# Optimization experiments

Measured on AMD Instinct MI355X. Metric: run time of the kernel, lower is better.

The kernel has to match this reference:

```python
import jax, jax.numpy as jnp
import numpy as np

HIDDEN = 1024
HEADS = 16
HEAD_DIM = HIDDEN // HEADS
EPS = 1e-5


def _layernorm(x, w, b):
    mu = jnp.mean(x, axis=-1, keepdims=True)
    var = jnp.mean(jnp.square(x - mu), axis=-1, keepdims=True)
    return (x - mu) * jax.lax.rsqrt(var + EPS) * w + b


def setup_inputs() -> dict:
    key = jax.random.key(0)
    ks = jax.random.split(key, 8)
    D = HIDDEN
    x = jax.random.normal(ks[0], (4, 4096, D), dtype=jnp.float32)
    s = 0.02
    return {
        "x": x,
        "qkv_w": jax.random.normal(ks[1], (3 * D, D), jnp.float32) * s,
        "qkv_b": jnp.zeros((3 * D,), jnp.float32),
        "proj_w": jax.random.normal(ks[2], (D, D), jnp.float32) * s,
        "proj_b": jnp.zeros((D,), jnp.float32),
        "ln1_w": jnp.ones((D,), jnp.float32),
        "ln1_b": jnp.zeros((D,), jnp.float32),
        "ln2_w": jnp.ones((D,), jnp.float32),
        "ln2_b": jnp.zeros((D,), jnp.float32),
        "mlp_w1": jax.random.normal(ks[3], (4 * D, D), jnp.float32) * s,
        "mlp_b1": jnp.zeros((4 * D,), jnp.float32),
        "mlp_w2": jax.random.normal(ks[4], (D, 4 * D), jnp.float32) * s,
        "mlp_b2": jnp.zeros((D,), jnp.float32),
    }


def reference(x, qkv_w, qkv_b, proj_w, proj_b, ln1_w, ln1_b, ln2_w, ln2_b,
              mlp_w1, mlp_b1, mlp_w2, mlp_b2):
    B, L, D = x.shape
    h = _layernorm(x, ln1_w, ln1_b)
    qkv = (h @ qkv_w.T + qkv_b).reshape(B, L, 3, HEADS, HEAD_DIM)
    q, k, v = qkv[:, :, 0], qkv[:, :, 1], qkv[:, :, 2]  # (B, L, H, hd)
    # NOTE: faithful to source - NO (L,H) transpose, so attention mixes
    # across the head axis per token: scores shape (B, L, H, H).
    attn = jnp.einsum('blhd,blgd->blhg', q, k) / np.sqrt(HEAD_DIM).astype(np.float32)
    attn = jax.nn.softmax(attn, axis=-1)
    out = jnp.einsum('blhg,blgd->blhd', attn, v).reshape(B, L, D)
    out = out @ proj_w.T + proj_b
    x = x + out
    h2 = _layernorm(x, ln2_w, ln2_b)
    mlp = jax.nn.gelu(h2 @ mlp_w1.T + mlp_b1, approximate=False) @ mlp_w2.T + mlp_b2
    return x + mlp
```

## Files before the change

kernel.cpp:

```cpp
#include <hip/hip_runtime.h>
#include <cstdint>
#include <cmath>


#define NTOK   16384
#define DMODEL 1024

typedef __bf16 bf16x8 __attribute__((ext_vector_type(8)));
typedef float  f32x4  __attribute__((ext_vector_type(4)));
typedef unsigned int __attribute__((address_space(1))) as1_uint;
typedef unsigned int __attribute__((address_space(3))) as3_uint;

__device__ __forceinline__ unsigned short f2bf(float f) {
    unsigned int u = __builtin_bit_cast(unsigned int, f);
    u += 0x7fffu + ((u >> 16) & 1u);
    return (unsigned short)(u >> 16);
}
__device__ __forceinline__ float bf2f(unsigned short s) {
    unsigned int u = ((unsigned int)s) << 16;
    return __builtin_bit_cast(float, u);
}

__device__ __forceinline__ void g2l16(const unsigned short* g, unsigned short* l) {
    __builtin_amdgcn_global_load_lds((const as1_uint*)g, (as3_uint*)l, 16, 0, 0);
}

__global__ __launch_bounds__(256) void cast_f32_bf16(
    const float4* __restrict__ in, ushort4* __restrict__ out, int n4) {
    int i = blockIdx.x * 256 + threadIdx.x;
    if (i < n4) {
        float4 v = in[i];
        ushort4 o;
        o.x = f2bf(v.x); o.y = f2bf(v.y); o.z = f2bf(v.z); o.w = f2bf(v.w);
        out[i] = o;
    }
}

__global__ __launch_bounds__(256) void ln_cast(
    const float* __restrict__ x, const float* __restrict__ w,
    const float* __restrict__ b, unsigned short* __restrict__ out) {
    int tok = blockIdx.x;
    int t   = threadIdx.x;
    float4 v = ((const float4*)x)[tok * 256 + t];
    float s  = v.x + v.y + v.z + v.w;
    float ss = v.x * v.x + v.y * v.y + v.z * v.z + v.w * v.w;
    #pragma unroll
    for (int off = 32; off > 0; off >>= 1) {
        s  += __shfl_down(s, off);
        ss += __shfl_down(ss, off);
    }
    __shared__ float red[8];
    int wave = t >> 6;
    if ((t & 63) == 0) { red[wave * 2] = s; red[wave * 2 + 1] = ss; }
    __syncthreads();
    s  = red[0] + red[2] + red[4] + red[6];
    ss = red[1] + red[3] + red[5] + red[7];
    float mu  = s * (1.0f / 1024.0f);
    float var = ss * (1.0f / 1024.0f) - mu * mu;
    float rs  = rsqrtf(var + 1e-5f);
    float4 wv = ((const float4*)w)[t];
    float4 bv = ((const float4*)b)[t];
    ushort4 o;
    o.x = f2bf((v.x - mu) * rs * wv.x + bv.x);
    o.y = f2bf((v.y - mu) * rs * wv.y + bv.y);
    o.z = f2bf((v.z - mu) * rs * wv.z + bv.z);
    o.w = f2bf((v.w - mu) * rs * wv.w + bv.w);
    ((ushort4*)out)[tok * 256 + t] = o;
}

__global__ __launch_bounds__(256) void attn_heads(
    const unsigned short* __restrict__ qkv, unsigned short* __restrict__ out) {
    __shared__ float sQ[1024], sK[1024], sV[1024];
    __shared__ float sS[256];
    int tok = blockIdx.x;
    int t   = threadIdx.x;
    const unsigned short* base = qkv + (size_t)tok * 3072;
    for (int i = t; i < 1024; i += 256) {
        sQ[i] = bf2f(base[i]);
        sK[i] = bf2f(base[1024 + i]);
        sV[i] = bf2f(base[2048 + i]);
    }
    __syncthreads();
    {
        int h = t >> 4, g = t & 15;
        float s = 0.0f;
        #pragma unroll
        for (int d = 0; d < 64; ++d) s += sQ[h * 64 + d] * sK[g * 64 + d];
        sS[h * 16 + g] = s * 0.125f;
    }
    __syncthreads();
    if (t < 16) {
        float mx = -1e30f;
        for (int g = 0; g < 16; ++g) mx = fmaxf(mx, sS[t * 16 + g]);
        float sum = 0.0f;
        for (int g = 0; g < 16; ++g) {
            float e = expf(sS[t * 16 + g] - mx);
            sS[t * 16 + g] = e;
            sum += e;
        }
        float inv = 1.0f / sum;
        for (int g = 0; g < 16; ++g) sS[t * 16 + g] *= inv;
    }
    __syncthreads();
    #pragma unroll
    for (int j = 0; j < 4; ++j) {
        int o = t + 256 * j;
        int h = o >> 6, d = o & 63;
        float s = 0.0f;
        #pragma unroll
        for (int g = 0; g < 16; ++g) s += sS[h * 16 + g] * sV[g * 64 + d];
        out[(size_t)tok * 1024 + o] = f2bf(s);
    }
}

#define BM 128
#define BN 128

template <int EPI>
__global__ __launch_bounds__(256) void gemm_bf16(
    const unsigned short* __restrict__ A, const unsigned short* __restrict__ W,
    const float* __restrict__ bias, const float* resid, void* Cout,
    int M, int N, int K) {
    __shared__ __align__(16) unsigned short As[2 * 128 * 32];
    __shared__ __align__(16) unsigned short Bs[2 * 128 * 32];

    const int t    = threadIdx.x;
    const int lane = t & 63;
    const int wave = t >> 6;
    const int wm   = wave >> 1;
    const int wn   = wave & 1;

    const int gm = M >> 7, gn = N >> 7;
    int m0, n0;
    if ((gm & 7) == 0) {
        const int xcd = blockIdx.x & 7;
        const int lid = blockIdx.x >> 3;
        const int mX  = gm >> 3;
        const int nsub   = lid & 7;
        const int t2     = lid >> 3;
        const int mloc   = t2 % mX;
        const int npanel = t2 / mX;
        m0 = (xcd * mX + mloc) << 7;
        n0 = (npanel * 8 + nsub) << 7;
    } else {
        m0 = (blockIdx.x / gn) << 7;
        n0 = (blockIdx.x % gn) << 7;
    }

    const int rw = wave * 32 + (lane >> 2);
    const int cg = (lane & 3) ^ ((lane >> 3) & 3);
    const unsigned short* gA0 = A + (size_t)(m0 + rw) * K + cg * 8;
    const unsigned short* gA1 = gA0 + (size_t)16 * K;
    const unsigned short* gB0 = W + (size_t)(n0 + rw) * K + cg * 8;
    const unsigned short* gB1 = gB0 + (size_t)16 * K;
    unsigned short* lA0 = As + (wave * 2 + 0) * 512;
    unsigned short* lA1 = As + (wave * 2 + 1) * 512;
    unsigned short* lB0 = Bs + (wave * 2 + 0) * 512;
    unsigned short* lB1 = Bs + (wave * 2 + 1) * 512;

    const int fr  = lane & 15;
    const int fq  = lane >> 4;
    const int csw = fq ^ ((fr >> 1) & 3);

    f32x4 acc[4][4] = {};

    for (int k0 = 0; k0 < K; k0 += 64) {
        __syncthreads();
        g2l16(gA0 + k0,      lA0);
        g2l16(gA1 + k0,      lA1);
        g2l16(gB0 + k0,      lB0);
        g2l16(gB1 + k0,      lB1);
        g2l16(gA0 + k0 + 32, lA0 + 4096);
        g2l16(gA1 + k0 + 32, lA1 + 4096);
        g2l16(gB0 + k0 + 32, lB0 + 4096);
        g2l16(gB1 + k0 + 32, lB1 + 4096);
        __syncthreads();

        #pragma unroll
        for (int kk = 0; kk < 2; ++kk) {
            bf16x8 af[4], bf[4];
            #pragma unroll
            for (int i = 0; i < 4; ++i)
                af[i] = *(const bf16x8*)(As + kk * 4096 +
                                         (wm * 64 + i * 16 + fr) * 32 + csw * 8);
            #pragma unroll
            for (int i = 0; i < 4; ++i)
                bf[i] = *(const bf16x8*)(Bs + kk * 4096 +
                                         (wn * 64 + i * 16 + fr) * 32 + csw * 8);
            #pragma unroll
            for (int im = 0; im < 4; ++im)
                #pragma unroll
                for (int in = 0; in < 4; ++in)
                    acc[im][in] = __builtin_amdgcn_mfma_f32_16x16x32_bf16(
                        af[im], bf[in], acc[im][in], 0, 0, 0);
        }
    }

    #pragma unroll
    for (int in = 0; in < 4; ++in) {
        int col = n0 + wn * 64 + in * 16 + fr;
        float bv = bias[col];
        #pragma unroll
        for (int im = 0; im < 4; ++im) {
            int rowb = m0 + wm * 64 + im * 16 + fq * 4;
            #pragma unroll
            for (int e = 0; e < 4; ++e) {
                size_t idx = (size_t)(rowb + e) * N + col;
                float v = acc[im][in][e] + bv;
                if (EPI == 0) {
                    ((unsigned short*)Cout)[idx] = f2bf(v);
                } else if (EPI == 1) {
                    ((float*)Cout)[idx] = v + resid[idx];
                } else {
                    float s  = 0.7978845608f * (v + 0.044715f * v * v * v);
                    float e2 = __expf(2.0f * s);
                    float th = 1.0f - 2.0f / (e2 + 1.0f);
                    ((unsigned short*)Cout)[idx] = f2bf(0.5f * v * (1.0f + th));
                }
            }
        }
    }
}

extern "C" void kernel_launch(void* const* d_in, const int* in_sizes, int n_in,
                              void* d_out, int out_size, void* d_ws, size_t ws_size,
                              hipStream_t stream) {
    const float* x      = (const float*)d_in[0];
    const float* qkv_w  = (const float*)d_in[1];
    const float* qkv_b  = (const float*)d_in[2];
    const float* proj_w = (const float*)d_in[3];
    const float* proj_b = (const float*)d_in[4];
    const float* ln1_w  = (const float*)d_in[5];
    const float* ln1_b  = (const float*)d_in[6];
    const float* ln2_w  = (const float*)d_in[7];
    const float* ln2_b  = (const float*)d_in[8];
    const float* mlp_w1 = (const float*)d_in[9];
    const float* mlp_b1 = (const float*)d_in[10];
    const float* mlp_w2 = (const float*)d_in[11];
    const float* mlp_b2 = (const float*)d_in[12];
    float* out = (float*)d_out;

    const size_t WB = 25165824;
    char* ws = (char*)d_ws;
    unsigned short* w_qkv  = (unsigned short*)(ws);
    unsigned short* w_proj = (unsigned short*)(ws + 6291456);
    unsigned short* w_m1   = (unsigned short*)(ws + 8388608);
    unsigned short* w_m2   = (unsigned short*)(ws + 16777216);

    int T = NTOK;
    while (T >= 256 && WB + (size_t)T * 12288 > ws_size) T >>= 1;
    if (T < 256) {
        hipMemcpyAsync(out, x, (size_t)NTOK * DMODEL * sizeof(float),
                       hipMemcpyDeviceToDevice, stream);
        return;
    }

    unsigned short* hbuf = (unsigned short*)(ws + WB);
    unsigned short* abuf = (unsigned short*)(ws + WB + (size_t)T * 2048);
    unsigned short* qmbuf= (unsigned short*)(ws + WB + (size_t)T * 4096);

    cast_f32_bf16<<<3072, 256, 0, stream>>>((const float4*)qkv_w,  (ushort4*)w_qkv,  786432);
    cast_f32_bf16<<<1024, 256, 0, stream>>>((const float4*)proj_w, (ushort4*)w_proj, 262144);
    cast_f32_bf16<<<4096, 256, 0, stream>>>((const float4*)mlp_w1, (ushort4*)w_m1,   1048576);
    cast_f32_bf16<<<4096, 256, 0, stream>>>((const float4*)mlp_w2, (ushort4*)w_m2,   1048576);

    for (int tok0 = 0; tok0 < NTOK; tok0 += T) {
        const float* xc   = x   + (size_t)tok0 * DMODEL;
        float*       outc = out + (size_t)tok0 * DMODEL;
        const int my = T / BM;

        ln_cast<<<T, 256, 0, stream>>>(xc, ln1_w, ln1_b, hbuf);
        gemm_bf16<0><<<(3072 / BN) * my, 256, 0, stream>>>(
            hbuf, w_qkv, qkv_b, nullptr, qmbuf, T, 3072, 1024);
        attn_heads<<<T, 256, 0, stream>>>(qmbuf, abuf);
        gemm_bf16<1><<<(1024 / BN) * my, 256, 0, stream>>>(
            abuf, w_proj, proj_b, xc, (void*)outc, T, 1024, 1024);
        ln_cast<<<T, 256, 0, stream>>>(outc, ln2_w, ln2_b, hbuf);
        gemm_bf16<2><<<(4096 / BN) * my, 256, 0, stream>>>(
            hbuf, w_m1, mlp_b1, nullptr, qmbuf, T, 4096, 1024);
        gemm_bf16<1><<<(1024 / BN) * my, 256, 0, stream>>>(
            qmbuf, w_m2, mlp_b2, outc, (void*)outc, T, 1024, 4096);
    }
}
```

Measured before the change: 1.023 ms.

## Restructure GEMM to 256x256 tiles with 8 waves and interleaved double-buffered prefetch

Replaces the 128x128, 4-wave bf16 GEMM with a 256x256 tile, 8-wave kernel. Global-to-LDS loads for the next K-step go into a second LDS buffer and are issued in halves between MFMA blocks, paced with s_waitcnt and barriers, and MFMA blocks raise wave priority. Block-to-XCD swizzling is generalized. The goal is more data reuse per byte loaded and overlap of memory traffic with MFMA compute. The cost is fewer workgroups per GEMM, which can hurt wave-count balance on the smaller N=1024 GEMMs, plus higher register pressure from the 8x4 accumulator tile.

```diff
diff --git a/kernel.cpp b/kernel.cpp
--- a/kernel.cpp
+++ b/kernel.cpp
@@ -23,6 +23,10 @@
 
 __device__ __forceinline__ void g2l16(const unsigned short* g, unsigned short* l) {
     __builtin_amdgcn_global_load_lds((const as1_uint*)g, (as3_uint*)l, 16, 0, 0);
+}
+
+__device__ __forceinline__ f32x4 mfma16(bf16x8 a, bf16x8 b, f32x4 c) {
+    return __builtin_amdgcn_mfma_f32_16x16x32_bf16(a, b, c, 0, 0, 0);
 }
 
 __global__ __launch_bounds__(256) void cast_f32_bf16(
@@ -113,100 +117,138 @@
     }
 }
 
-#define BM 128
-#define BN 128
+#define BM 256
+#define BN 256
+
+#define READ_A(kh) { _Pragma("unroll")                                        \
+    for (int mf = 0; mf < 8; ++mf)                                            \
+        a[mf] = *(const bf16x8*)(lA + bo + (kh)*8192 + pA + mf*512 + roA); }
+#define READ_B(kh, i0, i1) {                                                  \
+    b[i0] = *(const bf16x8*)(lB + bo + (kh)*8192 + pB + (i0)*512 + roB);      \
+    b[i1] = *(const bf16x8*)(lB + bo + (kh)*8192 + pB + (i1)*512 + roB); }
+#define MFMA_BLK(i0, i1) {                                                    \
+    __builtin_amdgcn_s_setprio(1);                                            \
+    _Pragma("unroll")                                                         \
+    for (int mf = 0; mf < 8; ++mf) {                                          \
+        acc[mf][i0] = mfma16(a[mf], b[i0], acc[mf][i0]);                      \
+        acc[mf][i1] = mfma16(a[mf], b[i1], acc[mf][i1]);                      \
+    }                                                                         \
+    __builtin_amdgcn_s_setprio(0); }
 
 template <int EPI>
-__global__ __launch_bounds__(256) void gemm_bf16(
+__global__ __launch_bounds__(512, 2) void gemm_bf16(
     const unsigned short* __restrict__ A, const unsigned short* __restrict__ W,
     const float* __restrict__ bias, const float* resid, void* Cout,
     int M, int N, int K) {
-    __shared__ __align__(16) unsigned short As[2 * 128 * 32];
-    __shared__ __align__(16) unsigned short Bs[2 * 128 * 32];
+    __shared__ __align__(16) unsigned short sA[2][4][4096];
+    __shared__ __align__(16) unsigned short sB[2][4][4096];
+    unsigned short* const lA = &sA[0][0][0];
+    unsigned short* const lB = &sB[0][0][0];
 
     const int t    = threadIdx.x;
     const int lane = t & 63;
-    const int wave = t >> 6;
-    const int wm   = wave >> 1;
-    const int wn   = wave & 1;
-
-    const int gm = M >> 7, gn = N >> 7;
-    int m0, n0;
-    if ((gm & 7) == 0) {
-        const int xcd = blockIdx.x & 7;
-        const int lid = blockIdx.x >> 3;
-        const int mX  = gm >> 3;
-        const int nsub   = lid & 7;
-        const int t2     = lid >> 3;
-        const int mloc   = t2 % mX;
-        const int npanel = t2 / mX;
-        m0 = (xcd * mX + mloc) << 7;
-        n0 = (npanel * 8 + nsub) << 7;
-    } else {
-        m0 = (blockIdx.x / gn) << 7;
-        n0 = (blockIdx.x % gn) << 7;
-    }
-
-    const int rw = wave * 32 + (lane >> 2);
-    const int cg = (lane & 3) ^ ((lane >> 3) & 3);
-    const unsigned short* gA0 = A + (size_t)(m0 + rw) * K + cg * 8;
-    const unsigned short* gA1 = gA0 + (size_t)16 * K;
-    const unsigned short* gB0 = W + (size_t)(n0 + rw) * K + cg * 8;
-    const unsigned short* gB1 = gB0 + (size_t)16 * K;
-    unsigned short* lA0 = As + (wave * 2 + 0) * 512;
-    unsigned short* lA1 = As + (wave * 2 + 1) * 512;
-    unsigned short* lB0 = Bs + (wave * 2 + 0) * 512;
-    unsigned short* lB1 = Bs + (wave * 2 + 1) * 512;
-
-    const int fr  = lane & 15;
-    const int fq  = lane >> 4;
-    const int csw = fq ^ ((fr >> 1) & 3);
-
-    f32x4 acc[4][4] = {};
-
-    for (int k0 = 0; k0 < K; k0 += 64) {
-        __syncthreads();
-        g2l16(gA0 + k0,      lA0);
-        g2l16(gA1 + k0,      lA1);
-        g2l16(gB0 + k0,      lB0);
-        g2l16(gB1 + k0,      lB1);
-        g2l16(gA0 + k0 + 32, lA0 + 4096);
-        g2l16(gA1 + k0 + 32, lA1 + 4096);
-        g2l16(gB0 + k0 + 32, lB0 + 4096);
-        g2l16(gB1 + k0 + 32, lB1 + 4096);
-        __syncthreads();
-
+    const int w    = t >> 6;
+    const int wm   = w >> 2;
+    const int wn   = w & 3;
+
+    const int gm = M >> 8, gn = N >> 8;
+    const int nwg = gm * gn;
+    int swz;
+    {
+        const int q = nwg >> 3, r = nwg & 7;
+        const int xcd = blockIdx.x & 7, lid = blockIdx.x >> 3;
+        swz = (xcd < r ? xcd * (q + 1) : r * (q + 1) + (xcd - r) * q) + lid;
+    }
+    const int m0 = (swz % gm) << 8;
+    const int n0 = (swz / gm) << 8;
+    (void)gn;
+
+    const int srow = w * 16 + (lane >> 2);
+    const int cg8  = ((lane & 3) ^ ((lane >> 3) & 3)) * 8;
+    const unsigned short* gA0 = A + (size_t)(m0 +       srow) * K + cg8;
+    const unsigned short* gA1 = A + (size_t)(m0 + 128 + srow) * K + cg8;
+    const unsigned short* gB0 = W + (size_t)(n0 +       srow) * K + cg8;
+    const unsigned short* gB1 = W + (size_t)(n0 + 128 + srow) * K + cg8;
+    const int wst = w * 512;
+
+    const int fr   = lane & 15, fq = lane >> 4;
+    const int csw8 = (fq ^ ((fr >> 1) & 3)) * 8;
+    const int roA  = fr * 32 + csw8;
+    const int roB  = (wn & 1) * 2048 + fr * 32 + csw8;
+    const int pA   = wm * 4096;
+    const int pB   = (wn >> 1) * 4096;
+
+    f32x4 acc[8][4] = {};
+
+    g2l16(gA0,      lA + 0 * 4096 + wst);
+    g2l16(gA1,      lA + 1 * 4096 + wst);
+    g2l16(gB0,      lB + 0 * 4096 + wst);
+    g2l16(gB1,      lB + 1 * 4096 + wst);
+    g2l16(gA0 + 32, lA + 2 * 4096 + wst);
+    g2l16(gA1 + 32, lA + 3 * 4096 + wst);
+    g2l16(gB0 + 32, lB + 2 * 4096 + wst);
+    g2l16(gB1 + 32, lB + 3 * 4096 + wst);
+    asm volatile("s_waitcnt vmcnt(4)" ::: "memory");
+    __builtin_amdgcn_s_barrier();
+
+    const int NT = K >> 6;
+    for (int kt = 0; kt < NT - 1; ++kt) {
+        const int bo = (kt & 1) << 14;
+        const int so = bo ^ 16384;
+        const size_t kg = (size_t)kt * 64 + 64;
+        bf16x8 a[8], b[4];
+
+        READ_A(0); READ_B(0, 0, 1);
+        g2l16(gA0 + kg, lA + so + wst);
+        g2l16(gA1 + kg, lA + so + 4096 + wst);
+        MFMA_BLK(0, 1);
+        __builtin_amdgcn_s_barrier();
+        READ_B(0, 2, 3);
+        g2l16(gB0 + kg, lB + so + wst);
+        g2l16(gB1 + kg, lB + so + 4096 + wst);
+        MFMA_BLK(2, 3);
+        asm volatile("s_waitcnt vmcnt(4)" ::: "memory");
+        __builtin_amdgcn_s_barrier();
+        READ_A(1); READ_B(1, 0, 1);
+        g2l16(gA0 + kg + 32, lA + so + 8192 + wst);
+        g2l16(gA1 + kg + 32, lA + so + 8192 + 4096 + wst);
+        MFMA_BLK(0, 1);
+        __builtin_amdgcn_s_barrier();
+        READ_B(1, 2, 3);
+        g2l16(gB0 + kg + 32, lB + so + 8192 + wst);
+        g2l16(gB1 + kg + 32, lB + so + 8192 + 4096 + wst);
+        MFMA_BLK(2, 3);
+        asm volatile("s_waitcnt vmcnt(4)" ::: "memory");
+        __builtin_amdgcn_s_barrier();
+    }
+
+    {
+        const int bo = ((NT - 1) & 1) << 14;
+        bf16x8 a[8], b[4];
+        READ_A(0); READ_B(0, 0, 1);
+        MFMA_BLK(0, 1);
+        __builtin_amdgcn_s_barrier();
+        READ_B(0, 2, 3);
+        MFMA_BLK(2, 3);
+        asm volatile("s_waitcnt vmcnt(0)" ::: "memory");
+        __builtin_amdgcn_s_barrier();
+        READ_A(1); READ_B(1, 0, 1);
+        MFMA_BLK(0, 1);
+        READ_B(1, 2, 3);
+        MFMA_BLK(2, 3);
+    }
+
+    #pragma unroll
+    for (int nf = 0; nf < 4; ++nf) {
+        const int col = n0 + wn * 64 + nf * 16 + fr;
+        const float bv = bias[col];
         #pragma unroll
-        for (int kk = 0; kk < 2; ++kk) {
-            bf16x8 af[4], bf[4];
-            #pragma unroll
-            for (int i = 0; i < 4; ++i)
-                af[i] = *(const bf16x8*)(As + kk * 4096 +
-                                         (wm * 64 + i * 16 + fr) * 32 + csw * 8);
-            #pragma unroll
-            for (int i = 0; i < 4; ++i)
-                bf[i] = *(const bf16x8*)(Bs + kk * 4096 +
-                                         (wn * 64 + i * 16 + fr) * 32 + csw * 8);
-            #pragma unroll
-            for (int im = 0; im < 4; ++im)
-                #pragma unroll
-                for (int in = 0; in < 4; ++in)
-                    acc[im][in] = __builtin_amdgcn_mfma_f32_16x16x32_bf16(
-                        af[im], bf[in], acc[im][in], 0, 0, 0);
-        }
-    }
-
-    #pragma unroll
-    for (int in = 0; in < 4; ++in) {
-        int col = n0 + wn * 64 + in * 16 + fr;
-        float bv = bias[col];
-        #pragma unroll
-        for (int im = 0; im < 4; ++im) {
-            int rowb = m0 + wm * 64 + im * 16 + fq * 4;
+        for (int mf = 0; mf < 8; ++mf) {
+            const int rowb = m0 + wm * 128 + mf * 16 + fq * 4;
             #pragma unroll
             for (int e = 0; e < 4; ++e) {
                 size_t idx = (size_t)(rowb + e) * N + col;
-                float v = acc[im][in][e] + bv;
+                float v = acc[mf][nf][e] + bv;
                 if (EPI == 0) {
                     ((unsigned short*)Cout)[idx] = f2bf(v);
                 } else if (EPI == 1) {
@@ -221,6 +263,10 @@
         }
     }
 }
+
+#undef READ_A
+#undef READ_B
+#undef MFMA_BLK
 
 extern "C" void kernel_launch(void* const* d_in, const int* in_sizes, int n_in,
                               void* d_out, int out_size, void* d_ws, size_t ws_size,
@@ -270,15 +316,15 @@
         const int my = T / BM;
 
         ln_cast<<<T, 256, 0, stream>>>(xc, ln1_w, ln1_b, hbuf);
-        gemm_bf16<0><<<(3072 / BN) * my, 256, 0, stream>>>(
+        gemm_bf16<0><<<(3072 / BN) * my, 512, 0, stream>>>(
             hbuf, w_qkv, qkv_b, nullptr, qmbuf, T, 3072, 1024);
         attn_heads<<<T, 256, 0, stream>>>(qmbuf, abuf);
-        gemm_bf16<1><<<(1024 / BN) * my, 256, 0, stream>>>(
+        gemm_bf16<1><<<(1024 / BN) * my, 512, 0, stream>>>(
             abuf, w_proj, proj_b, xc, (void*)outc, T, 1024, 1024);
         ln_cast<<<T, 256, 0, stream>>>(outc, ln2_w, ln2_b, hbuf);
-        gemm_bf16<2><<<(4096 / BN) * my, 256, 0, stream>>>(
+        gemm_bf16<2><<<(4096 / BN) * my, 512, 0, stream>>>(
             hbuf, w_m1, mlp_b1, nullptr, qmbuf, T, 4096, 1024);
-        gemm_bf16<1><<<(1024 / BN) * my, 256, 0, stream>>>(
+        gemm_bf16<1><<<(1024 / BN) * my, 512, 0, stream>>>(
             qmbuf, w_m2, mlp_b2, outc, (void*)outc, T, 1024, 4096);
     }
 }
```

Result: no change. 1.013 ms (-1.0%).
